# Kernel optimization log

Measured on AMD Instinct MI355X. Metric: run time of the kernel, lower is better.

## Reference

```python
import jax, jax.numpy as jnp
import numpy as np

LN10 = float(np.log(10.0))
EPS = 1e-10


def _band_e(L1, L2, R1, R2, rho1, rho2, g2p, g2m, gp, gm,
            cos1, sin1, cos2, sin2, epsexp, deltexp, epsdelexp):
    """EC-stage expected energy over the (tau, gamma) grid.
    L*,R*: (S,N) real; rho*: (S,N) complex -> (S, ntaus, ngammas)."""
    # first part: gamma-only terms (S,G) broadcast over taus
    first = (jnp.sum(L1 * L2, 1)[:, None] * g2p
             + jnp.sum(R1 * R2, 1)[:, None] * g2m) * epsexp
    first = first[:, None, :] + (jnp.sum(L1 * R2, 1)
                                 + jnp.sum(R1 * L2, 1))[:, None, None]
    r1r, r1i = jnp.real(rho1), jnp.imag(rho1)
    r2r, r2i = jnp.real(rho2), jnp.imag(rho2)
    # Re(rho * exp(-i*w*tau)) = Re(rho)*cos(w*tau) + Im(rho)*sin(w*tau);
    # contracting over the N frames first avoids the (S,N,ntaus) intermediate.
    sec = ((jnp.sum(L1 * r1r, 1) + jnp.sum(L2 * r2r, 1))[:, None] * cos1
           + (jnp.sum(L1 * r1i, 1) + jnp.sum(L2 * r2i, 1))[:, None] * sin1)  # (S,T)
    second = 2.0 * sec[:, :, None] * gp * epsdelexp[None]
    thr = ((jnp.sum(R1 * r1r, 1) + jnp.sum(R2 * r2r, 1))[:, None] * cos1
           + (jnp.sum(R1 * r1i, 1) + jnp.sum(R2 * r2i, 1))[:, None] * sin1)
    third = 2.0 * thr[:, :, None] * gm * epsdelexp[None]
    t1 = jnp.sum(r1r * r2r + r1i * r2i, 1)          # Re(sum rho1*conj(rho2)), (S,)
    q = jnp.sum(rho1 * rho2, 1)                     # (S,) complex
    t2 = jnp.real(q)[:, None] * cos2 + jnp.imag(q)[:, None] * sin2  # Re(q*e^{-2iwt})
    fourth = 2.0 * (t1[:, None] + deltexp[None, :] * t2)[:, :, None]
    return first - second - third + fourth


def _ec(xl_re, xl_im, xr_re, xr_im, yl_re, yl_im, yr_re, yr_im,
        cf, taus, gammas, sigma_epsilon, sigma_delta, fids, N):
    xl = xl_re + 1j * xl_im
    xr = xr_re + 1j * xr_im
    yl = yl_re + 1j * yl_im
    yr = yr_re + 1j * yr_im
    F = xl.shape[1]
    S = F - N + 1                                   # number of N-frame segments
    widx = jnp.arange(S)[:, None] + jnp.arange(N)[None, :]
    fids_np = np.asarray(fids)
    J = fids_np.shape[0]
    epsexp = jnp.exp(2.0 * LN10 ** 2 * sigma_epsilon ** 2)        # (G,)
    g2p, g2m = 10.0 ** (2.0 * gammas), 10.0 ** (-2.0 * gammas)    # (G,)
    gp, gm = 10.0 ** gammas, 10.0 ** (-gammas)
    d = []
    for i in range(J):                              # J=15 structurally distinct bands
        lo, hi = int(fids_np[i, 0]) - 1, int(fids_np[i, 1])
        c = cf[i]
        wt = c * taus
        cos1, sin1 = jnp.cos(wt), jnp.sin(wt)       # tauexp = cos - i*sin
        cos2, sin2 = jnp.cos(2.0 * wt), jnp.sin(2.0 * wt)
        deltexp = jnp.exp(-(c ** 2) * sigma_delta ** 2)           # (T,)
        epsdelexp = jnp.exp(0.5 * (LN10 ** 2 * sigma_epsilon[None, :] ** 2
                                   - (c ** 2) * sigma_delta[:, None] ** 2))  # (T,G)

        def seg(a):
            return a[lo:hi][:, widx]                # (kk,S,N) sliding windows

        def norm(s):
            L = jnp.sum(jnp.real(jnp.conj(s) * s), 0)             # (S,N)
            return L - L.mean(1, keepdims=True)

        def rho(sr, sl):
            r = jnp.sum(jnp.conj(sr) * sl, 0)                     # (S,N) complex
            return r - r.mean(1, keepdims=True)

        sxl, sxr, syl, syr = seg(xl), seg(xr), seg(yl), seg(yr)
        Lx, Rx, Ly, Ry = norm(sxl), norm(sxr), norm(syl), norm(syr)
        rhox, rhoy = rho(sxr, sxl), rho(syr, syl)
        args = (g2p, g2m, gp, gm, cos1, sin1, cos2, sin2, epsexp, deltexp, epsdelexp)
        exy = _band_e(Lx, Ly, Rx, Ry, rhoy, rhox, *args)
        exx = _band_e(Lx, Lx, Rx, Rx, rhox, rhox, *args)
        eyy = _band_e(Ly, Ly, Ry, Ry, rhoy, rhoy, *args)
        p = exy / jnp.sqrt(jnp.maximum(exx * eyy, EPS))
        d.append(jnp.max(p.reshape(S, -1), axis=1))               # max over (tau,gamma)
    return jnp.stack(d, 0)                                        # (J,S)


def setup_inputs() -> dict:
    key = jax.random.key(0)
    K, F, N, J, T, G = 128, 4000, 30, 15, 100, 40
    ks = jax.random.split(key, 8)
    names = ["xl_re", "xl_im", "xr_re", "xr_im", "yl_re", "yl_im", "yr_re", "yr_im"]
    inp = {n: 0.1 * jax.random.normal(k, (K, F), dtype=jnp.float32)
           for n, k in zip(names, ks)}
    edges = np.array([0, 3, 5, 8, 11, 15, 20, 26, 33, 41, 50, 61, 74, 89, 107, 128])
    fids = np.stack([edges[:-1] + 1, edges[1:]], axis=1).astype(np.int64)  # 1-based
    cf = 2.0 * np.pi * np.geomspace(150.0, 4000.0, J)   # centre freqs in rad/s
    taus = np.linspace(-1e-3, 1e-3, T)
    gammas = np.linspace(-1.0, 1.0, G)                  # dB/20 units
    sigma_delta = 65e-6 * (1.0 + np.abs(taus) / 1e-3)
    sigma_epsilon = np.sqrt(2.0) * (1.5 / 20.0) * (1.0 + np.abs(gammas))
    inp.update(
        cf=jnp.asarray(cf, jnp.float32),
        taus=jnp.asarray(taus, jnp.float32),
        gammas=jnp.asarray(gammas, jnp.float32),
        sigma_epsilon=jnp.asarray(sigma_epsilon, jnp.float32),
        sigma_delta=jnp.asarray(sigma_delta, jnp.float32),
        fids=jnp.asarray(fids),
        N=N,
    )
    return inp


def reference(xl_re, xl_im, xr_re, xr_im, yl_re, yl_im, yr_re, yr_im,
              cf, taus, gammas, sigma_epsilon, sigma_delta, fids, N):
    return _ec(xl_re, xl_im, xr_re, xr_im, yl_re, yl_im, yr_re, yr_im,
               cf, taus, gammas, sigma_epsilon, sigma_delta, fids, N)
```

## Files before the change

### kernel.cpp

```cpp
#include <hip/hip_runtime.h>
#include <math.h>

#define LN10_SQ 5.3018981104783984f
#define LOG2_10 3.3219280948873623f

constexpr int NWIN = 30;
constexpr int SEGS_PER_BLOCK = 64;
constexpr int NF = SEGS_PER_BLOCK + NWIN - 1;
constexpr int TSPLIT = 4;

__global__ __launch_bounds__(256, 4) void ec_fused_kernel(
    const float* __restrict__ xlr, const float* __restrict__ xli,
    const float* __restrict__ xrre, const float* __restrict__ xrim,
    const float* __restrict__ ylr, const float* __restrict__ yli,
    const float* __restrict__ yrre, const float* __restrict__ yrim,
    const float* __restrict__ cf, const float* __restrict__ taus,
    const float* __restrict__ gammas, const float* __restrict__ sigeps,
    const float* __restrict__ sigdel, const int* __restrict__ fids,
    float* __restrict__ out, int F, int S, int T, int G, int K)
{
    __shared__ float4 ttabA[128];
    __shared__ float2 ttabB[128];
    __shared__ float4 gtab[64];
    __shared__ float  sser[8][96];
    __shared__ float  red[256];

    const int tid = threadIdx.x;
    const int band = blockIdx.y;
    const int seg_base = blockIdx.x * SEGS_PER_BLOCK;
    const float cw = cf[band];

    int lo, hi;
    if (fids[1] == 0) {
        lo = fids[4 * band] - 1;
        hi = fids[4 * band + 2];
    } else {
        lo = fids[2 * band] - 1;
        hi = fids[2 * band + 1];
    }
    lo = lo < 0 ? 0 : lo;
    hi = hi > K ? K : hi;

    {
        int gg = tid - 100;
        if (gg >= 0 && gg < G) {
            float gam = gammas[gg];
            float se = sigeps[gg];
            float ee = expf(2.0f * LN10_SQ * se * se);
            float Eg = expf(0.5f * LN10_SQ * se * se);
            float g2p = exp2f(2.0f * gam * LOG2_10);
            float g2m = exp2f(-2.0f * gam * LOG2_10);
            float gp = exp2f(gam * LOG2_10);
            float gm = exp2f(-gam * LOG2_10);
            gtab[gg] = make_float4(g2p * ee, g2m * ee, gp * Eg, gm * Eg);
        }
        int tt = tid - 156;
        if (tt >= 0 && tt < T) {
            float tau = taus[tt];
            float wt = cw * tau;
            float sn1, cs1, sn2, cs2;
            sincosf(wt, &sn1, &cs1);
            sincosf(2.0f * wt, &sn2, &cs2);
            float sd = sigdel[tt];
            float Dt = expf(-0.5f * cw * cw * sd * sd);
            ttabA[tt] = make_float4(cs1, sn1, cs2, sn2);
            ttabB[tt] = make_float2(2.0f * Dt, 2.0f * Dt * Dt);
        }
    }

    for (int j = tid; j < NF; j += 256) {
        int f = seg_base + j;
        float Lx = 0.f, Rx = 0.f, Ly = 0.f, Ry = 0.f;
        float rxr = 0.f, rxi = 0.f, ryr = 0.f, ryi = 0.f;
        if (f < F) {
            for (int k = lo; k < hi; ++k) {
                int idx = k * F + f;
                float a = xlr[idx], b = xli[idx], c = xrre[idx], d = xrim[idx];
                Lx = fmaf(a, a, fmaf(b, b, Lx));
                Rx = fmaf(c, c, fmaf(d, d, Rx));
                rxr = fmaf(c, a, fmaf(d, b, rxr));
                rxi = fmaf(c, b, rxi) - d * a;
                float e = ylr[idx], g = yli[idx], h = yrre[idx], i2 = yrim[idx];
                Ly = fmaf(e, e, fmaf(g, g, Ly));
                Ry = fmaf(h, h, fmaf(i2, i2, Ry));
                ryr = fmaf(h, e, fmaf(i2, g, ryr));
                ryi = fmaf(h, g, ryi) - i2 * e;
            }
        }
        sser[0][j] = Lx;  sser[1][j] = Rx;
        sser[2][j] = Ly;  sser[3][j] = Ry;
        sser[4][j] = rxr; sser[5][j] = rxi;
        sser[6][j] = ryr; sser[7][j] = ryi;
    }
    __syncthreads();

    const int segL = tid & (SEGS_PER_BLOCK - 1);
    const int split = tid >> 6;

    float s0=0,s1=0,s2=0,s3=0,s4=0,s5=0,s6=0,s7=0;
    float c00=0,c01=0,c02=0,c03=0,c04=0,c05=0,c06=0,c07=0;
    float c11=0,c12=0,c13=0,c14=0,c15=0,c16=0,c17=0;
    float c22=0,c23=0,c24=0,c25=0,c26=0,c27=0;
    float c33=0,c34=0,c35=0,c36=0,c37=0;
    float c44=0,c45=0,c46=0,c47=0;
    float c55=0,c56=0,c57=0;
    float c66=0,c67=0;
    float c77=0;
    #pragma unroll 5
    for (int n = 0; n < NWIN; ++n) {
        float v0 = sser[0][segL + n], v1 = sser[1][segL + n];
        float v2 = sser[2][segL + n], v3 = sser[3][segL + n];
        float v4 = sser[4][segL + n], v5 = sser[5][segL + n];
        float v6 = sser[6][segL + n], v7 = sser[7][segL + n];
        s0+=v0; s1+=v1; s2+=v2; s3+=v3; s4+=v4; s5+=v5; s6+=v6; s7+=v7;
        c00=fmaf(v0,v0,c00); c01=fmaf(v0,v1,c01); c02=fmaf(v0,v2,c02); c03=fmaf(v0,v3,c03);
        c04=fmaf(v0,v4,c04); c05=fmaf(v0,v5,c05); c06=fmaf(v0,v6,c06); c07=fmaf(v0,v7,c07);
        c11=fmaf(v1,v1,c11); c12=fmaf(v1,v2,c12); c13=fmaf(v1,v3,c13); c14=fmaf(v1,v4,c14);
        c15=fmaf(v1,v5,c15); c16=fmaf(v1,v6,c16); c17=fmaf(v1,v7,c17);
        c22=fmaf(v2,v2,c22); c23=fmaf(v2,v3,c23); c24=fmaf(v2,v4,c24); c25=fmaf(v2,v5,c25);
        c26=fmaf(v2,v6,c26); c27=fmaf(v2,v7,c27);
        c33=fmaf(v3,v3,c33); c34=fmaf(v3,v4,c34); c35=fmaf(v3,v5,c35); c36=fmaf(v3,v6,c36);
        c37=fmaf(v3,v7,c37);
        c44=fmaf(v4,v4,c44); c45=fmaf(v4,v5,c45); c46=fmaf(v4,v6,c46); c47=fmaf(v4,v7,c47);
        c55=fmaf(v5,v5,c55); c56=fmaf(v5,v6,c56); c57=fmaf(v5,v7,c57);
        c66=fmaf(v6,v6,c66); c67=fmaf(v6,v7,c67);
        c77=fmaf(v7,v7,c77);
    }

    const float rN = 1.0f / (float)NWIN;
    #define CEN(a,b) fmaf(-(s##a * rN), s##b, c##a##b)

    float t46 = CEN(4,6), t57 = CEN(5,7), t56 = CEN(5,6), t47 = CEN(4,7);
    float A_xy = CEN(0,2), B_xy = CEN(1,3);
    float base_xy = CEN(0,3) + CEN(1,2) + 2.0f * (t46 + t57);
    float sc_xy = CEN(0,6) + CEN(2,4), ss_xy = CEN(0,7) + CEN(2,5);
    float tc_xy = CEN(1,6) + CEN(3,4), ts_xy = CEN(1,7) + CEN(3,5);
    float qr_xy = t46 - t57, qi_xy = t56 + t47;
    float t44 = CEN(4,4), t55 = CEN(5,5);
    float A_xx = CEN(0,0), B_xx = CEN(1,1);
    float base_xx = 2.0f * CEN(0,1) + 2.0f * (t44 + t55);
    float sc_xx = 2.0f * CEN(0,4), ss_xx = 2.0f * CEN(0,5);
    float tc_xx = 2.0f * CEN(1,4), ts_xx = 2.0f * CEN(1,5);
    float qr_xx = t44 - t55, qi_xx = 2.0f * CEN(4,5);
    float t66 = CEN(6,6), t77 = CEN(7,7);
    float A_yy = CEN(2,2), B_yy = CEN(3,3);
    float base_yy = 2.0f * CEN(2,3) + 2.0f * (t66 + t77);
    float sc_yy = 2.0f * CEN(2,6), ss_yy = 2.0f * CEN(2,7);
    float tc_yy = 2.0f * CEN(3,6), ts_yy = 2.0f * CEN(3,7);
    float qr_yy = t66 - t77, qi_yy = 2.0f * CEN(6,7);
    #undef CEN

    const int tlen = (T + TSPLIT - 1) / TSPLIT;
    const int tstart = split * tlen;
    const int tend = (tstart + tlen < T) ? (tstart + tlen) : T;
    float m = -3.4e38f;
    for (int t = tstart; t < tend; ++t) {
        float4 ta = ttabA[t];
        float2 tb = ttabB[t];
        float w_xy = fmaf(tb.y, fmaf(qi_xy, ta.w, qr_xy * ta.z), base_xy);
        float ud_xy = fmaf(ss_xy, ta.y, sc_xy * ta.x) * tb.x;
        float vd_xy = fmaf(ts_xy, ta.y, tc_xy * ta.x) * tb.x;
        float w_xx = fmaf(tb.y, fmaf(qi_xx, ta.w, qr_xx * ta.z), base_xx);
        float ud_xx = fmaf(ss_xx, ta.y, sc_xx * ta.x) * tb.x;
        float vd_xx = fmaf(ts_xx, ta.y, tc_xx * ta.x) * tb.x;
        float w_yy = fmaf(tb.y, fmaf(qi_yy, ta.w, qr_yy * ta.z), base_yy);
        float ud_yy = fmaf(ss_yy, ta.y, sc_yy * ta.x) * tb.x;
        float vd_yy = fmaf(ts_yy, ta.y, tc_yy * ta.x) * tb.x;
        #pragma unroll 4
        for (int g = 0; g < G; ++g) {
            float4 gt = gtab[g];
            float exy = fmaf(A_xy, gt.x, w_xy);
            exy = fmaf(B_xy, gt.y, exy);
            exy = fmaf(-ud_xy, gt.z, exy);
            exy = fmaf(-vd_xy, gt.w, exy);
            float exx = fmaf(A_xx, gt.x, w_xx);
            exx = fmaf(B_xx, gt.y, exx);
            exx = fmaf(-ud_xx, gt.z, exx);
            exx = fmaf(-vd_xx, gt.w, exx);
            float eyy = fmaf(A_yy, gt.x, w_yy);
            eyy = fmaf(B_yy, gt.y, eyy);
            eyy = fmaf(-ud_yy, gt.z, eyy);
            eyy = fmaf(-vd_yy, gt.w, eyy);
            float den = fmaxf(exx * eyy, 1e-10f);
            float p = exy * __builtin_amdgcn_rsqf(den);
            m = fmaxf(m, p);
        }
    }

    red[tid] = m;
    __syncthreads();
    if (tid < SEGS_PER_BLOCK) {
        float r = fmaxf(fmaxf(red[tid], red[tid + 64]),
                        fmaxf(red[tid + 128], red[tid + 192]));
        int seg = seg_base + tid;
        if (seg < S) out[(size_t)band * S + seg] = r;
    }
}

extern "C" void kernel_launch(void* const* d_in, const int* in_sizes, int n_in,
                              void* d_out, int out_size, void* d_ws, size_t ws_size,
                              hipStream_t stream) {
    const float* xlr  = (const float*)d_in[0];
    const float* xli  = (const float*)d_in[1];
    const float* xrre = (const float*)d_in[2];
    const float* xrim = (const float*)d_in[3];
    const float* ylr  = (const float*)d_in[4];
    const float* yli  = (const float*)d_in[5];
    const float* yrre = (const float*)d_in[6];
    const float* yrim = (const float*)d_in[7];
    const float* cfp  = (const float*)d_in[8];
    const float* taus = (const float*)d_in[9];
    const float* gammas = (const float*)d_in[10];
    const float* sigeps = (const float*)d_in[11];
    const float* sigdel = (const float*)d_in[12];
    const int*   fids = (const int*)d_in[13];

    const int J = in_sizes[8];
    const int T = in_sizes[9];
    const int G = in_sizes[10];
    const int S = out_size / J;
    const int F = S + NWIN - 1;
    const int K = in_sizes[0] / F;

    dim3 b(256), g((S + SEGS_PER_BLOCK - 1) / SEGS_PER_BLOCK, J);
    ec_fused_kernel<<<g, b, 0, stream>>>(xlr, xli, xrre, xrim,
                                         ylr, yli, yrre, yrim,
                                         cfp, taus, gammas, sigeps, sigdel,
                                         fids, (float*)d_out, F, S, T, G, K);
}
```

Before: 127.5 us.

## Compute window covariances once per segment and split tau grid across 512 threads

The block grows to 512 threads and the tau range is split eight ways instead of four, so each thread runs a shorter tau×gamma inner loop. The 30-frame covariance accumulation, which every T-split thread used to redo, is now done once by 64 threads, and its 27 derived scalars go through shared memory. The tau bounds are made wave-uniform with readfirstlane. The trade-off is an extra barrier, idle threads during the covariance phase, more shared memory, and higher register pressure under launch_bounds(512,8).

After: 126.3 us. About the same (-1.0%).

```diff
diff --git a/kernel.cpp b/kernel.cpp
--- a/kernel.cpp
+++ b/kernel.cpp
@@ -6,10 +6,11 @@
 
 constexpr int NWIN = 30;
 constexpr int SEGS_PER_BLOCK = 64;
-constexpr int NF = SEGS_PER_BLOCK + NWIN - 1;
-constexpr int TSPLIT = 4;
-
-__global__ __launch_bounds__(256, 4) void ec_fused_kernel(
+constexpr int NFRM = SEGS_PER_BLOCK + NWIN - 1;
+constexpr int NTHREADS = 512;
+constexpr int TSPLIT = 8;
+
+__global__ __launch_bounds__(NTHREADS, 8) void ec_fused_kernel(
     const float* __restrict__ xlr, const float* __restrict__ xli,
     const float* __restrict__ xrre, const float* __restrict__ xrim,
     const float* __restrict__ ylr, const float* __restrict__ yli,
@@ -23,7 +24,8 @@
     __shared__ float2 ttabB[128];
     __shared__ float4 gtab[64];
     __shared__ float  sser[8][96];
-    __shared__ float  red[256];
+    __shared__ float  scal[27][64];
+    __shared__ float  red[NTHREADS];
 
     const int tid = threadIdx.x;
     const int band = blockIdx.y;
@@ -42,7 +44,19 @@
     hi = hi > K ? K : hi;
 
     {
-        int gg = tid - 100;
+        int tt = tid - 128;
+        if (tt >= 0 && tt < T) {
+            float tau = taus[tt];
+            float wt = cw * tau;
+            float sn1, cs1, sn2, cs2;
+            sincosf(wt, &sn1, &cs1);
+            sincosf(2.0f * wt, &sn2, &cs2);
+            float sd = sigdel[tt];
+            float Dt = expf(-0.5f * cw * cw * sd * sd);
+            ttabA[tt] = make_float4(cs1, sn1, cs2, sn2);
+            ttabB[tt] = make_float2(2.0f * Dt, 2.0f * Dt * Dt);
+        }
+        int gg = tid - 256;
         if (gg >= 0 && gg < G) {
             float gam = gammas[gg];
             float se = sigeps[gg];
@@ -54,21 +68,10 @@
             float gm = exp2f(-gam * LOG2_10);
             gtab[gg] = make_float4(g2p * ee, g2m * ee, gp * Eg, gm * Eg);
         }
-        int tt = tid - 156;
-        if (tt >= 0 && tt < T) {
-            float tau = taus[tt];
-            float wt = cw * tau;
-            float sn1, cs1, sn2, cs2;
-            sincosf(wt, &sn1, &cs1);
-            sincosf(2.0f * wt, &sn2, &cs2);
-            float sd = sigdel[tt];
-            float Dt = expf(-0.5f * cw * cw * sd * sd);
-            ttabA[tt] = make_float4(cs1, sn1, cs2, sn2);
-            ttabB[tt] = make_float2(2.0f * Dt, 2.0f * Dt * Dt);
-        }
-    }
-
-    for (int j = tid; j < NF; j += 256) {
+    }
+
+    if (tid < NFRM) {
+        int j = tid;
         int f = seg_base + j;
         float Lx = 0.f, Rx = 0.f, Ly = 0.f, Ry = 0.f;
         float rxr = 0.f, rxi = 0.f, ryr = 0.f, ryi = 0.f;
@@ -94,65 +97,91 @@
     }
     __syncthreads();
 
-    const int segL = tid & (SEGS_PER_BLOCK - 1);
+    if (tid < SEGS_PER_BLOCK) {
+        const int segL = tid;
+        float s0=0,s1=0,s2=0,s3=0,s4=0,s5=0,s6=0,s7=0;
+        float c00=0,c01=0,c02=0,c03=0,c04=0,c05=0,c06=0,c07=0;
+        float c11=0,c12=0,c13=0,c14=0,c15=0,c16=0,c17=0;
+        float c22=0,c23=0,c24=0,c25=0,c26=0,c27=0;
+        float c33=0,c34=0,c35=0,c36=0,c37=0;
+        float c44=0,c45=0,c46=0,c47=0;
+        float c55=0,c56=0,c57=0;
+        float c66=0,c67=0;
+        float c77=0;
+        #pragma unroll 5
+        for (int n = 0; n < NWIN; ++n) {
+            float v0 = sser[0][segL + n], v1 = sser[1][segL + n];
+            float v2 = sser[2][segL + n], v3 = sser[3][segL + n];
+            float v4 = sser[4][segL + n], v5 = sser[5][segL + n];
+            float v6 = sser[6][segL + n], v7 = sser[7][segL + n];
+            s0+=v0; s1+=v1; s2+=v2; s3+=v3; s4+=v4; s5+=v5; s6+=v6; s7+=v7;
+            c00=fmaf(v0,v0,c00); c01=fmaf(v0,v1,c01); c02=fmaf(v0,v2,c02); c03=fmaf(v0,v3,c03);
+            c04=fmaf(v0,v4,c04); c05=fmaf(v0,v5,c05); c06=fmaf(v0,v6,c06); c07=fmaf(v0,v7,c07);
+            c11=fmaf(v1,v1,c11); c12=fmaf(v1,v2,c12); c13=fmaf(v1,v3,c13); c14=fmaf(v1,v4,c14);
+            c15=fmaf(v1,v5,c15); c16=fmaf(v1,v6,c16); c17=fmaf(v1,v7,c17);
+            c22=fmaf(v2,v2,c22); c23=fmaf(v2,v3,c23); c24=fmaf(v2,v4,c24); c25=fmaf(v2,v5,c25);
+            c26=fmaf(v2,v6,c26); c27=fmaf(v2,v7,c27);
+            c33=fmaf(v3,v3,c33); c34=fmaf(v3,v4,c34); c35=fmaf(v3,v5,c35); c36=fmaf(v3,v6,c36);
+            c37=fmaf(v3,v7,c37);
+            c44=fmaf(v4,v4,c44); c45=fmaf(v4,v5,c45); c46=fmaf(v4,v6,c46); c47=fmaf(v4,v7,c47);
+            c55=fmaf(v5,v5,c55); c56=fmaf(v5,v6,c56); c57=fmaf(v5,v7,c57);
+            c66=fmaf(v6,v6,c66); c67=fmaf(v6,v7,c67);
+            c77=fmaf(v7,v7,c77);
+        }
+        const float rN = 1.0f / (float)NWIN;
+        #define CEN(a,b) fmaf(-(s##a * rN), s##b, c##a##b)
+        float t46 = CEN(4,6), t57 = CEN(5,7), t56 = CEN(5,6), t47 = CEN(4,7);
+        scal[0][segL] = CEN(0,2);
+        scal[1][segL] = CEN(1,3);
+        scal[2][segL] = CEN(0,3) + CEN(1,2) + 2.0f*(t46+t57);
+        scal[3][segL] = CEN(0,6) + CEN(2,4);
+        scal[4][segL] = CEN(0,7) + CEN(2,5);
+        scal[5][segL] = CEN(1,6) + CEN(3,4);
+        scal[6][segL] = CEN(1,7) + CEN(3,5);
+        scal[7][segL] = t46 - t57;
+        scal[8][segL] = t56 + t47;
+        float t44 = CEN(4,4), t55 = CEN(5,5);
+        scal[9][segL]  = CEN(0,0);
+        scal[10][segL] = CEN(1,1);
+        scal[11][segL] = 2.0f*CEN(0,1) + 2.0f*(t44+t55);
+        scal[12][segL] = 2.0f*CEN(0,4);
+        scal[13][segL] = 2.0f*CEN(0,5);
+        scal[14][segL] = 2.0f*CEN(1,4);
+        scal[15][segL] = 2.0f*CEN(1,5);
+        scal[16][segL] = t44 - t55;
+        scal[17][segL] = 2.0f*CEN(4,5);
+        float t66 = CEN(6,6), t77 = CEN(7,7);
+        scal[18][segL] = CEN(2,2);
+        scal[19][segL] = CEN(3,3);
+        scal[20][segL] = 2.0f*CEN(2,3) + 2.0f*(t66+t77);
+        scal[21][segL] = 2.0f*CEN(2,6);
+        scal[22][segL] = 2.0f*CEN(2,7);
+        scal[23][segL] = 2.0f*CEN(3,6);
+        scal[24][segL] = 2.0f*CEN(3,7);
+        scal[25][segL] = t66 - t77;
+        scal[26][segL] = 2.0f*CEN(6,7);
+        #undef CEN
+    }
+    __syncthreads();
+
+    const int seg = tid & (SEGS_PER_BLOCK - 1);
     const int split = tid >> 6;
-
-    float s0=0,s1=0,s2=0,s3=0,s4=0,s5=0,s6=0,s7=0;
-    float c00=0,c01=0,c02=0,c03=0,c04=0,c05=0,c06=0,c07=0;
-    float c11=0,c12=0,c13=0,c14=0,c15=0,c16=0,c17=0;
-    float c22=0,c23=0,c24=0,c25=0,c26=0,c27=0;
-    float c33=0,c34=0,c35=0,c36=0,c37=0;
-    float c44=0,c45=0,c46=0,c47=0;
-    float c55=0,c56=0,c57=0;
-    float c66=0,c67=0;
-    float c77=0;
-    #pragma unroll 5
-    for (int n = 0; n < NWIN; ++n) {
-        float v0 = sser[0][segL + n], v1 = sser[1][segL + n];
-        float v2 = sser[2][segL + n], v3 = sser[3][segL + n];
-        float v4 = sser[4][segL + n], v5 = sser[5][segL + n];
-        float v6 = sser[6][segL + n], v7 = sser[7][segL + n];
-        s0+=v0; s1+=v1; s2+=v2; s3+=v3; s4+=v4; s5+=v5; s6+=v6; s7+=v7;
-        c00=fmaf(v0,v0,c00); c01=fmaf(v0,v1,c01); c02=fmaf(v0,v2,c02); c03=fmaf(v0,v3,c03);
-        c04=fmaf(v0,v4,c04); c05=fmaf(v0,v5,c05); c06=fmaf(v0,v6,c06); c07=fmaf(v0,v7,c07);
-        c11=fmaf(v1,v1,c11); c12=fmaf(v1,v2,c12); c13=fmaf(v1,v3,c13); c14=fmaf(v1,v4,c14);
-        c15=fmaf(v1,v5,c15); c16=fmaf(v1,v6,c16); c17=fmaf(v1,v7,c17);
-        c22=fmaf(v2,v2,c22); c23=fmaf(v2,v3,c23); c24=fmaf(v2,v4,c24); c25=fmaf(v2,v5,c25);
-        c26=fmaf(v2,v6,c26); c27=fmaf(v2,v7,c27);
-        c33=fmaf(v3,v3,c33); c34=fmaf(v3,v4,c34); c35=fmaf(v3,v5,c35); c36=fmaf(v3,v6,c36);
-        c37=fmaf(v3,v7,c37);
-        c44=fmaf(v4,v4,c44); c45=fmaf(v4,v5,c45); c46=fmaf(v4,v6,c46); c47=fmaf(v4,v7,c47);
-        c55=fmaf(v5,v5,c55); c56=fmaf(v5,v6,c56); c57=fmaf(v5,v7,c57);
-        c66=fmaf(v6,v6,c66); c67=fmaf(v6,v7,c67);
-        c77=fmaf(v7,v7,c77);
-    }
-
-    const float rN = 1.0f / (float)NWIN;
-    #define CEN(a,b) fmaf(-(s##a * rN), s##b, c##a##b)
-
-    float t46 = CEN(4,6), t57 = CEN(5,7), t56 = CEN(5,6), t47 = CEN(4,7);
-    float A_xy = CEN(0,2), B_xy = CEN(1,3);
-    float base_xy = CEN(0,3) + CEN(1,2) + 2.0f * (t46 + t57);
-    float sc_xy = CEN(0,6) + CEN(2,4), ss_xy = CEN(0,7) + CEN(2,5);
-    float tc_xy = CEN(1,6) + CEN(3,4), ts_xy = CEN(1,7) + CEN(3,5);
-    float qr_xy = t46 - t57, qi_xy = t56 + t47;
-    float t44 = CEN(4,4), t55 = CEN(5,5);
-    float A_xx = CEN(0,0), B_xx = CEN(1,1);
-    float base_xx = 2.0f * CEN(0,1) + 2.0f * (t44 + t55);
-    float sc_xx = 2.0f * CEN(0,4), ss_xx = 2.0f * CEN(0,5);
-    float tc_xx = 2.0f * CEN(1,4), ts_xx = 2.0f * CEN(1,5);
-    float qr_xx = t44 - t55, qi_xx = 2.0f * CEN(4,5);
-    float t66 = CEN(6,6), t77 = CEN(7,7);
-    float A_yy = CEN(2,2), B_yy = CEN(3,3);
-    float base_yy = 2.0f * CEN(2,3) + 2.0f * (t66 + t77);
-    float sc_yy = 2.0f * CEN(2,6), ss_yy = 2.0f * CEN(2,7);
-    float tc_yy = 2.0f * CEN(3,6), ts_yy = 2.0f * CEN(3,7);
-    float qr_yy = t66 - t77, qi_yy = 2.0f * CEN(6,7);
-    #undef CEN
-
-    const int tlen = (T + TSPLIT - 1) / TSPLIT;
-    const int tstart = split * tlen;
-    const int tend = (tstart + tlen < T) ? (tstart + tlen) : T;
+    const float A_xy = scal[0][seg],  B_xy = scal[1][seg],  base_xy = scal[2][seg];
+    const float sc_xy = scal[3][seg], ss_xy = scal[4][seg];
+    const float tc_xy = scal[5][seg], ts_xy = scal[6][seg];
+    const float qr_xy = scal[7][seg], qi_xy = scal[8][seg];
+    const float A_xx = scal[9][seg],  B_xx = scal[10][seg], base_xx = scal[11][seg];
+    const float sc_xx = scal[12][seg], ss_xx = scal[13][seg];
+    const float tc_xx = scal[14][seg], ts_xx = scal[15][seg];
+    const float qr_xx = scal[16][seg], qi_xx = scal[17][seg];
+    const float A_yy = scal[18][seg], B_yy = scal[19][seg], base_yy = scal[20][seg];
+    const float sc_yy = scal[21][seg], ss_yy = scal[22][seg];
+    const float tc_yy = scal[23][seg], ts_yy = scal[24][seg];
+    const float qr_yy = scal[25][seg], qi_yy = scal[26][seg];
+
+    const int tstart = __builtin_amdgcn_readfirstlane((split * T) / TSPLIT);
+    const int tend   = __builtin_amdgcn_readfirstlane(((split + 1) * T) / TSPLIT);
+
     float m = -3.4e38f;
     for (int t = tstart; t < tend; ++t) {
         float4 ta = ttabA[t];
@@ -190,10 +219,12 @@
     red[tid] = m;
     __syncthreads();
     if (tid < SEGS_PER_BLOCK) {
-        float r = fmaxf(fmaxf(red[tid], red[tid + 64]),
-                        fmaxf(red[tid + 128], red[tid + 192]));
-        int seg = seg_base + tid;
-        if (seg < S) out[(size_t)band * S + seg] = r;
+        float r = red[tid];
+        #pragma unroll
+        for (int kk = 1; kk < TSPLIT; ++kk)
+            r = fmaxf(r, red[tid + 64 * kk]);
+        int sg = seg_base + tid;
+        if (sg < S) out[(size_t)band * S + sg] = r;
     }
 }
 
@@ -222,7 +253,7 @@
     const int F = S + NWIN - 1;
     const int K = in_sizes[0] / F;
 
-    dim3 b(256), g((S + SEGS_PER_BLOCK - 1) / SEGS_PER_BLOCK, J);
+    dim3 b(NTHREADS), g((S + SEGS_PER_BLOCK - 1) / SEGS_PER_BLOCK, J);
     ec_fused_kernel<<<g, b, 0, stream>>>(xlr, xli, xrre, xrim,
                                          ylr, yli, yrre, yrim,
                                          cfp, taus, gammas, sigeps, sigdel,
```
